# Optimization experiments

Hardware: AMD Instinct MI355X
Metric: run time of the kernel (lower is better)

## Reference

```python
import jax, jax.numpy as jnp
import numpy as np

DIM = 256; DIM_HEAD = 32; HEADS = DIM // DIM_HEAD; WSZ = 8; D4 = DIM // 4
EPS = 1e-5
SCALE = DIM_HEAD ** -0.5


def _rel_pos_indices(wsz):
    pos = np.arange(wsz)
    grid = np.stack(np.meshgrid(pos, pos, indexing='ij')).reshape(2, -1).T  # (w*w, 2)
    rel = grid[:, None] - grid[None, :] + wsz - 1
    return jnp.asarray((rel * np.array([2 * wsz - 1, 1])).sum(-1))  # (w*w, w*w)


def _ln(x, g, b):
    m = x.mean(-1, keepdims=True)
    v = jnp.var(x, axis=-1, keepdims=True)
    return (x - m) / jnp.sqrt(v + EPS) * g + b


def setup_inputs() -> dict:
    key = jax.random.key(0)
    ks = jax.random.split(key, 8)
    inner = HEADS * DIM_HEAD
    def n(k, shape, s=0.02):
        return jax.random.normal(k, shape, dtype=jnp.float32) * s
    return {
        "x": jax.random.normal(ks[0], (2, DIM, 256, 256), dtype=jnp.float32),
        "norm_g": jnp.ones((1, DIM, 1, 1), jnp.float32),
        "norm_b": jnp.zeros((1, DIM, 1, 1), jnp.float32),
        "w_qkv": n(ks[1], (3 * inner, DIM)),
        "w_out": n(ks[2], (DIM, inner)),
        "b_out": jnp.zeros((DIM,), jnp.float32),
        "dpb_w1": n(ks[3], (D4, 2), 0.5), "dpb_b1": jnp.zeros((D4,), jnp.float32),
        "dpb_g1": jnp.ones((D4,), jnp.float32), "dpb_beta1": jnp.zeros((D4,), jnp.float32),
        "dpb_w2": n(ks[4], (D4, D4), 0.1), "dpb_b2": jnp.zeros((D4,), jnp.float32),
        "dpb_g2": jnp.ones((D4,), jnp.float32), "dpb_beta2": jnp.zeros((D4,), jnp.float32),
        "dpb_w3": n(ks[5], (D4, D4), 0.1), "dpb_b3": jnp.zeros((D4,), jnp.float32),
        "dpb_g3": jnp.ones((D4,), jnp.float32), "dpb_beta3": jnp.zeros((D4,), jnp.float32),
        "dpb_w4": n(ks[6], (1, D4), 0.1), "dpb_b4": jnp.zeros((1,), jnp.float32),
    }


def reference(x, norm_g, norm_b, w_qkv, w_out, b_out,
              dpb_w1, dpb_b1, dpb_g1, dpb_beta1,
              dpb_w2, dpb_b2, dpb_g2, dpb_beta2,
              dpb_w3, dpb_b3, dpb_g3, dpb_beta3,
              dpb_w4, dpb_b4):
    B, D, H, W = x.shape
    nh, nw = H // WSZ, W // WSZ
    # channel-first LayerNorm (stats over dim=1, biased variance)
    mean = x.mean(axis=1, keepdims=True)
    var = jnp.var(x, axis=1, keepdims=True)
    xn = (x - mean) / jnp.sqrt(var + EPS) * norm_g + norm_b
    # 'short' windowing: b d (h s1) (w s2) -> (b h w) d (s1 s2)
    xw = xn.reshape(B, D, nh, WSZ, nw, WSZ).transpose(0, 2, 4, 1, 3, 5)
    xw = xw.reshape(B * nh * nw, D, WSZ * WSZ)
    # 1x1 conv QKV == matmul over channel dim
    qkv = jnp.einsum('ed,bdn->ben', w_qkv, xw)
    q, k, v = jnp.split(qkv, 3, axis=1)
    to_heads = lambda t: t.reshape(-1, HEADS, DIM_HEAD, WSZ * WSZ).transpose(0, 1, 3, 2)
    q, k, v = to_heads(q) * SCALE, to_heads(k), to_heads(v)
    sim = jnp.einsum('bhid,bhjd->bhij', q, k)  # [Bw, H, 64, 64]
    # dynamic position bias MLP over relative coordinates in [-wsz, wsz]
    pos = jnp.arange(-WSZ, WSZ + 1, dtype=x.dtype)
    rel = jnp.stack(jnp.meshgrid(pos, pos, indexing='ij')).reshape(2, -1).T  # ((2w+1)^2, 2)
    h1 = jax.nn.relu(_ln(rel @ dpb_w1.T + dpb_b1, dpb_g1, dpb_beta1))
    h2 = jax.nn.relu(_ln(h1 @ dpb_w2.T + dpb_b2, dpb_g2, dpb_beta2))
    h3 = jax.nn.relu(_ln(h2 @ dpb_w3.T + dpb_b3, dpb_g3, dpb_beta3))
    biases = (h3 @ dpb_w4.T + dpb_b4)[:, 0]
    sim = sim + biases[_rel_pos_indices(WSZ)]
    attn = jax.nn.softmax(sim, axis=-1)
    out = jnp.einsum('bhij,bhjd->bhid', attn, v)
    # b h (x y) d -> b (h d) (x y)
    out = out.transpose(0, 1, 3, 2).reshape(-1, HEADS * DIM_HEAD, WSZ * WSZ)
    out = jnp.einsum('de,ben->bdn', w_out, out) + b_out[None, :, None]
    # (b h w) d s1 s2 -> b d (h s1) (w s2)
    out = out.reshape(B, nh, nw, D, WSZ, WSZ).transpose(0, 3, 1, 4, 2, 5).reshape(B, D, H, W)
    return out
```

## Files before the change

kernel.cpp:

```cpp
#include <hip/hip_runtime.h>


typedef __attribute__((ext_vector_type(8))) short bf16x8;
typedef __attribute__((ext_vector_type(4))) short bf16x4;
typedef __attribute__((ext_vector_type(4))) float f32x4;

#define LOG2E    1.44269504088896f
#define QK_SCALE 0.17677669529663687f

__device__ __forceinline__ short f2b(float f) {
  union { float f; unsigned u; } v; v.f = f;
  unsigned r = v.u + 0x7FFFu + ((v.u >> 16) & 1u);
  return (short)(r >> 16);
}

__device__ __forceinline__ unsigned pk2(float a, float b) {
  union { float f; unsigned u; } ua, ub; ua.f = a; ub.f = b;
#if __has_builtin(__builtin_amdgcn_perm)
  return __builtin_amdgcn_perm(ub.u + 0x8000u, ua.u + 0x8000u, 0x07060302u);
#else
  return ((ua.u + 0x8000u) >> 16) | ((ub.u + 0x8000u) & 0xFFFF0000u);
#endif
}

__device__ __forceinline__ bf16x8 mk8(unsigned a, unsigned b, unsigned c, unsigned d) {
  union { unsigned u[4]; bf16x8 v; } x; x.u[0] = a; x.u[1] = b; x.u[2] = c; x.u[3] = d;
  return x.v;
}
__device__ __forceinline__ bf16x4 mk4(unsigned a, unsigned b) {
  union { unsigned u[2]; bf16x4 v; } x; x.u[0] = a; x.u[1] = b; return x.v;
}

__device__ __forceinline__ f32x4 mfma16(bf16x4 a, bf16x4 b, f32x4 c) {
#if __has_builtin(__builtin_amdgcn_mfma_f32_16x16x16bf16_1k)
  return __builtin_amdgcn_mfma_f32_16x16x16bf16_1k(a, b, c, 0, 0, 0);
#else
  f32x4 d;
  asm volatile("v_mfma_f32_16x16x16_bf16 %0, %1, %2, %3"
               : "=&v"(d) : "v"(a), "v"(b), "v"(c));
  return d;
#endif
}

__device__ __forceinline__ float wave_sum64(float v) {
  v += __shfl_xor(v, 1);  v += __shfl_xor(v, 2);  v += __shfl_xor(v, 4);
  v += __shfl_xor(v, 8);  v += __shfl_xor(v, 16); v += __shfl_xor(v, 32);
  return v;
}

__global__ __launch_bounds__(256)
void prep_kernel(const float* __restrict__ wqkv, const float* __restrict__ wout,
                 const float* __restrict__ w1, const float* __restrict__ b1,
                 const float* __restrict__ g1, const float* __restrict__ be1,
                 const float* __restrict__ w2, const float* __restrict__ b2,
                 const float* __restrict__ g2, const float* __restrict__ be2,
                 const float* __restrict__ w3, const float* __restrict__ b3,
                 const float* __restrict__ g3, const float* __restrict__ be3,
                 const float* __restrict__ w4, const float* __restrict__ b4,
                 short* __restrict__ wq_t, short* __restrict__ wo_t,
                 float* __restrict__ sb) {
  __shared__ float h[64];
  __shared__ float wbuf[4096];

  if (blockIdx.x < 128) {
    int t = (blockIdx.x * 256 + threadIdx.x) * 8;
    if (t < 196608) {
      int blk = t >> 9, l = (t & 511) >> 3;
      int et = blk >> 3, kt = blk & 7;
      int e = et * 16 + (l & 15);
      int d = kt * 32 + (l >> 4) * 8;
      const float* src = wqkv + e * 256 + d;
      float sc = (e < 256) ? QK_SCALE * LOG2E : 1.0f;
      bf16x8 pk;
      #pragma unroll
      for (int el = 0; el < 8; ++el) pk[el] = f2b(src[el] * sc);
      *(bf16x8*)(wq_t + t) = pk;
    } else {
      int o = t - 196608;
      int blk = o >> 9, l = (o & 511) >> 3;
      int dt = blk >> 3, kt = blk & 7;
      int dout = dt * 16 + (l & 15);
      int e = kt * 32 + (l >> 4) * 8;
      const float* src = wout + dout * 256 + e;
      bf16x8 pk;
      #pragma unroll
      for (int el = 0; el < 8; ++el) pk[el] = f2b(src[el]);
      *(bf16x8*)(wo_t + o) = pk;
    }
    return;
  }

  if (threadIdx.x >= 64) return;
  const int f = threadIdx.x;
  const int pos = blockIdx.x - 128;
  const float py = (float)(pos / 17) - 8.0f;
  const float px = (float)(pos % 17) - 8.0f;

  float a = py * w1[2 * f] + px * w1[2 * f + 1] + b1[f];
  {
    float m = wave_sum64(a) * (1.f / 64.f);
    float d = a - m;
    float var = wave_sum64(d * d) * (1.f / 64.f);
    a = fmaxf(d * rsqrtf(var + 1e-5f) * g1[f] + be1[f], 0.f);
  }
  h[f] = a;
  __threadfence_block();

  #pragma unroll 8
  for (int k = 0; k < 64; ++k) wbuf[k * 64 + f] = w2[k * 64 + f];
  __threadfence_block();
  float acc = b2[f];
  #pragma unroll 8
  for (int k = 0; k < 64; ++k) {
    int g = (k + f) & 63;
    acc += wbuf[f * 64 + g] * h[g];
  }
  {
    float m = wave_sum64(acc) * (1.f / 64.f);
    float d = acc - m;
    float var = wave_sum64(d * d) * (1.f / 64.f);
    acc = fmaxf(d * rsqrtf(var + 1e-5f) * g2[f] + be2[f], 0.f);
  }
  __threadfence_block();
  h[f] = acc;
  __threadfence_block();

  #pragma unroll 8
  for (int k = 0; k < 64; ++k) wbuf[k * 64 + f] = w3[k * 64 + f];
  __threadfence_block();
  float acc3 = b3[f];
  #pragma unroll 8
  for (int k = 0; k < 64; ++k) {
    int g = (k + f) & 63;
    acc3 += wbuf[f * 64 + g] * h[g];
  }
  {
    float m = wave_sum64(acc3) * (1.f / 64.f);
    float d = acc3 - m;
    float var = wave_sum64(d * d) * (1.f / 64.f);
    acc3 = fmaxf(d * rsqrtf(var + 1e-5f) * g3[f] + be3[f], 0.f);
  }
  float o = wave_sum64(w4[f] * acc3);
  if (f == 0) sb[pos] = o + b4[0];
}

__global__ __launch_bounds__(512)
void expand_kernel(const float* __restrict__ sb, float* __restrict__ tblf) {
  int idx = blockIdx.x * 512 + threadIdx.x;
  int it = idx >> 10, jt = (idx >> 8) & 3, ln = (idx >> 2) & 63, jj = idx & 3;
  int rr = ln & 15, gg = ln >> 4;
  int i = it * 16 + rr;
  int j = jt * 16 + gg * 4 + jj;
  int dy = (i >> 3) - (j >> 3) + 7;
  int dx = (i & 7) - (j & 7) + 7;
  tblf[idx] = sb[dy * 15 + dx] * LOG2E;
}

#define SM_XA   0
#define SM_PS   65536
#define SM_SIZE 73728
#define XASWZ(p) ((((p) & 7) << 4) ^ ((((p) >> 3) & 3) << 7))

__global__ __launch_bounds__(512)
void attn_kernel(const float* __restrict__ x, const float* __restrict__ gnorm,
                 const float* __restrict__ bnorm, const short* __restrict__ wq_t,
                 const short* __restrict__ wo_t, const float* __restrict__ bout,
                 const float* __restrict__ tblf, float* __restrict__ out) {
  __shared__ __align__(16) char smem[SM_SIZE];
  const int t = threadIdx.x;
  const int lane = t & 63;
  const int w = t >> 6;
  const int r = lane & 15;
  const int gq = lane >> 4;

  const int bid = blockIdx.x;
  const int b   = bid >> 9;
  const int wh  = (bid >> 4) & 31;
  const int ww2 = bid & 15;
  const int R = wh * 8, C = ww2 * 16;

  const int n = lane;
  const int d0 = w * 32;
  float* PS = (float*)(smem + SM_PS);
  float xv[2][32];
  #pragma unroll
  for (int h = 0; h < 2; ++h) {
    const float* xb = x + (((size_t)(b * 256 + d0)) << 16) +
                      (R + 4 * h + (n >> 4)) * 256 + C + (n & 15);
    float s1 = 0.f, s2v = 0.f;
    #pragma unroll
    for (int i = 0; i < 32; ++i) {
      float v = xb[(size_t)i << 16];
      xv[h][i] = v; s1 += v; s2v += v * v;
    }
    PS[h * 1024 + w * 64 + n] = s1;
    PS[h * 1024 + 512 + w * 64 + n] = s2v;
  }
  __syncthreads();
  #pragma unroll
  for (int h = 0; h < 2; ++h) {
    float a = 0.f, q2 = 0.f;
    #pragma unroll
    for (int dg = 0; dg < 8; ++dg) {
      a  += PS[h * 1024 + dg * 64 + n];
      q2 += PS[h * 1024 + 512 + dg * 64 + n];
    }
    float mean = a * (1.f / 256.f);
    float var = q2 * (1.f / 256.f) - mean * mean;
    float rstd = rsqrtf(var + 1e-5f);
    int p2 = (4 * h + (n >> 4)) * 16 + (n & 15);
    #pragma unroll
    for (int c = 0; c < 4; ++c) {
      float xn[8];
      #pragma unroll
      for (int e = 0; e < 8; ++e) {
        int d = d0 + c * 8 + e;
        xn[e] = (xv[h][c * 8 + e] - mean) * rstd * gnorm[d] + bnorm[d];
      }
      *(bf16x8*)(smem + SM_XA + (p2 << 9) + ((((d0 + c * 8) << 1)) ^ XASWZ(p2))) =
          mk8(pk2(xn[0], xn[1]), pk2(xn[2], xn[3]), pk2(xn[4], xn[5]), pk2(xn[6], xn[7]));
    }
  }
  __syncthreads();

  const f32x4 vzero = {0.f, 0.f, 0.f, 0.f};

  f32x4 o2[2][2][4];
  float pinv[2][4];
  #pragma unroll
  for (int wl = 0; wl < 2; ++wl) {
    bf16x4 kpk[2][4], qpk[2][4];
    {
      f32x4 aq[2][4], ak[2][4];
      #pragma unroll
      for (int nt = 0; nt < 2; ++nt)
        #pragma unroll
        for (int t4 = 0; t4 < 4; ++t4) { aq[nt][t4] = vzero; ak[nt][t4] = vzero; }
      __builtin_amdgcn_s_setprio(1);
      #pragma unroll
      for (int kt = 0; kt < 8; ++kt) {
        bf16x8 bq0 = *(const bf16x8*)(wq_t + ((((0 * 16 + w * 2 + 0) * 8 + kt) << 9) + lane * 8));
        bf16x8 bq1 = *(const bf16x8*)(wq_t + ((((0 * 16 + w * 2 + 1) * 8 + kt) << 9) + lane * 8));
        bf16x8 bk0 = *(const bf16x8*)(wq_t + ((((1 * 16 + w * 2 + 0) * 8 + kt) << 9) + lane * 8));
        bf16x8 bk1 = *(const bf16x8*)(wq_t + ((((1 * 16 + w * 2 + 1) * 8 + kt) << 9) + lane * 8));
        bf16x8 afr[4];
        #pragma unroll
        for (int t4 = 0; t4 < 4; ++t4) {
          int p2 = (t4 * 2 + (r >> 3)) * 16 + wl * 8 + (r & 7);
          afr[t4] = *(const bf16x8*)(smem + SM_XA + (p2 << 9) + ((((kt * 32 + gq * 8) << 1)) ^ XASWZ(p2)));
        }
        #pragma unroll
        for (int t4 = 0; t4 < 4; ++t4) {
          aq[0][t4] = __builtin_amdgcn_mfma_f32_16x16x32_bf16(bq0, afr[t4], aq[0][t4], 0, 0, 0);
          aq[1][t4] = __builtin_amdgcn_mfma_f32_16x16x32_bf16(bq1, afr[t4], aq[1][t4], 0, 0, 0);
          ak[0][t4] = __builtin_amdgcn_mfma_f32_16x16x32_bf16(bk0, afr[t4], ak[0][t4], 0, 0, 0);
          ak[1][t4] = __builtin_amdgcn_mfma_f32_16x16x32_bf16(bk1, afr[t4], ak[1][t4], 0, 0, 0);
        }
      }
      __builtin_amdgcn_s_setprio(0);
      #pragma unroll
      for (int kb = 0; kb < 2; ++kb)
        #pragma unroll
        for (int t4 = 0; t4 < 4; ++t4) {
          qpk[kb][t4] = mk4(pk2(aq[kb][t4][0], aq[kb][t4][1]),
                            pk2(aq[kb][t4][2], aq[kb][t4][3]));
          kpk[kb][t4] = mk4(pk2(ak[kb][t4][0], ak[kb][t4][1]),
                            pk2(ak[kb][t4][2], ak[kb][t4][3]));
        }
    }
    bf16x4 va8[4][2];
    {
      f32x4 vacc[4][2];
      #pragma unroll
      for (int mt = 0; mt < 4; ++mt)
        #pragma unroll
        for (int nt = 0; nt < 2; ++nt) vacc[mt][nt] = vzero;
      __builtin_amdgcn_s_setprio(1);
      #pragma unroll
      for (int kt = 0; kt < 8; ++kt) {
        bf16x8 bfr0 = *(const bf16x8*)(wq_t + ((((2 * 16 + w * 2 + 0) * 8 + kt) << 9) + lane * 8));
        bf16x8 bfr1 = *(const bf16x8*)(wq_t + ((((2 * 16 + w * 2 + 1) * 8 + kt) << 9) + lane * 8));
        bf16x8 afr[4];
        #pragma unroll
        for (int mt = 0; mt < 4; ++mt) {
          int p2 = (mt * 2 + (r >> 3)) * 16 + wl * 8 + (r & 7);
          afr[mt] = *(const bf16x8*)(smem + SM_XA + (p2 << 9) + ((((kt * 32 + gq * 8) << 1)) ^ XASWZ(p2)));
        }
        #pragma unroll
        for (int mt = 0; mt < 4; ++mt) {
          vacc[mt][0] = __builtin_amdgcn_mfma_f32_16x16x32_bf16(afr[mt], bfr0, vacc[mt][0], 0, 0, 0);
          vacc[mt][1] = __builtin_amdgcn_mfma_f32_16x16x32_bf16(afr[mt], bfr1, vacc[mt][1], 0, 0, 0);
        }
      }
      __builtin_amdgcn_s_setprio(0);
      #pragma unroll
      for (int mt = 0; mt < 4; ++mt)
        #pragma unroll
        for (int nt = 0; nt < 2; ++nt)
          va8[mt][nt] = mk4(pk2(vacc[mt][nt][0], vacc[mt][nt][1]),
                            pk2(vacc[mt][nt][2], vacc[mt][nt][3]));
    }

    #pragma unroll
    for (int nt = 0; nt < 2; ++nt)
      #pragma unroll
      for (int it = 0; it < 4; ++it) o2[wl][nt][it] = vzero;
    __builtin_amdgcn_s_setprio(1);
    #pragma unroll
    for (int it = 0; it < 4; ++it) {
      f32x4 sc[4];
      #pragma unroll
      for (int jt = 0; jt < 4; ++jt) {
        sc[jt] = mfma16(kpk[0][jt], qpk[0][it], vzero);
        sc[jt] = mfma16(kpk[1][jt], qpk[1][it], sc[jt]);
      }
      float sum = 0.f;
      #pragma unroll
      for (int jt = 0; jt < 4; ++jt) {
        f32x4 bj = *(const f32x4*)(tblf + (((it * 4 + jt) * 64 + lane) << 2));
        #pragma unroll
        for (int jj = 0; jj < 4; ++jj) {
          float e = exp2f(sc[jt][jj] + bj[jj]);
          sc[jt][jj] = e; sum += e;
        }
      }
      sum += __shfl_xor(sum, 16);
      sum += __shfl_xor(sum, 32);
      pinv[wl][it] = 1.0f / sum;
      bf16x4 ppk[4];
      #pragma unroll
      for (int jt = 0; jt < 4; ++jt)
        ppk[jt] = mk4(pk2(sc[jt][0], sc[jt][1]), pk2(sc[jt][2], sc[jt][3]));
      #pragma unroll
      for (int mt = 0; mt < 4; ++mt)
        #pragma unroll
        for (int nt = 0; nt < 2; ++nt)
          o2[wl][nt][it] = mfma16(va8[mt][nt], ppk[mt], o2[wl][nt][it]);
    }
    __builtin_amdgcn_s_setprio(0);
  }
  __syncthreads();

  float bov[2];
  bov[0] = bout[w * 32 + r];
  bov[1] = bout[w * 32 + 16 + r];
  bf16x8 woB[2][8];
  #pragma unroll
  for (int nt = 0; nt < 2; ++nt)
    #pragma unroll
    for (int kt = 0; kt < 8; ++kt)
      woB[nt][kt] = *(const bf16x8*)(wo_t + ((((w * 2 + nt) * 8 + kt) << 9) + lane * 8));

  #pragma unroll
  for (int wl = 0; wl < 2; ++wl)
    #pragma unroll
    for (int nt = 0; nt < 2; ++nt)
      #pragma unroll
      for (int it = 0; it < 4; ++it) {
        float pv = pinv[wl][it];
        int pw = it * 16 + r;
        int p2 = ((pw >> 3) << 4) + (wl << 3) + (pw & 7);
        int e = (w << 5) + (nt << 4) + (gq << 2);
        *(bf16x4*)(smem + SM_XA + (p2 << 9) + (((e << 1)) ^ XASWZ(p2))) =
            mk4(pk2(o2[wl][nt][it][0] * pv, o2[wl][nt][it][1] * pv),
                pk2(o2[wl][nt][it][2] * pv, o2[wl][nt][it][3] * pv));
      }
  __syncthreads();

  #pragma unroll 1
  for (int ck = 0; ck < 2; ++ck) {
    f32x4 c3[4][2];
    #pragma unroll
    for (int mt = 0; mt < 4; ++mt)
      #pragma unroll
      for (int nt = 0; nt < 2; ++nt) c3[mt][nt] = vzero;
    __builtin_amdgcn_s_setprio(1);
    #pragma unroll
    for (int kt = 0; kt < 8; ++kt) {
      bf16x8 af[4];
      #pragma unroll
      for (int mt = 0; mt < 4; ++mt) {
        int p2 = ck * 64 + mt * 16 + r;
        af[mt] = *(const bf16x8*)(smem + SM_XA + (p2 << 9) + ((((kt * 32 + gq * 8) << 1)) ^ XASWZ(p2)));
      }
      #pragma unroll
      for (int mt = 0; mt < 4; ++mt)
        #pragma unroll
        for (int nt = 0; nt < 2; ++nt)
          c3[mt][nt] = __builtin_amdgcn_mfma_f32_16x16x32_bf16(af[mt], woB[nt][kt], c3[mt][nt], 0, 0, 0);
    }
    __builtin_amdgcn_s_setprio(0);
    #pragma unroll
    for (int mt = 0; mt < 4; ++mt)
      #pragma unroll
      for (int nt = 0; nt < 2; ++nt) {
        int dout = w * 32 + nt * 16 + r;
        int row = ck * 4 + mt;
        f32x4 v = c3[mt][nt];
        v[0] += bov[nt]; v[1] += bov[nt]; v[2] += bov[nt]; v[3] += bov[nt];
        *(f32x4*)(out + (((size_t)(b * 256 + dout)) << 16) + (R + row) * 256 + C + gq * 4) = v;
      }
  }
}

extern "C" void kernel_launch(void* const* d_in, const int* in_sizes, int n_in,
                              void* d_out, int out_size, void* d_ws, size_t ws_size,
                              hipStream_t stream) {
  const float* x     = (const float*)d_in[0];
  const float* gnorm = (const float*)d_in[1];
  const float* bnorm = (const float*)d_in[2];
  const float* wqkv  = (const float*)d_in[3];
  const float* wout  = (const float*)d_in[4];
  const float* bout  = (const float*)d_in[5];
  const float* w1  = (const float*)d_in[6];
  const float* b1  = (const float*)d_in[7];
  const float* g1  = (const float*)d_in[8];
  const float* be1 = (const float*)d_in[9];
  const float* w2  = (const float*)d_in[10];
  const float* b2  = (const float*)d_in[11];
  const float* g2  = (const float*)d_in[12];
  const float* be2 = (const float*)d_in[13];
  const float* w3  = (const float*)d_in[14];
  const float* b3  = (const float*)d_in[15];
  const float* g3  = (const float*)d_in[16];
  const float* be3 = (const float*)d_in[17];
  const float* w4  = (const float*)d_in[18];
  const float* b4  = (const float*)d_in[19];

  short* wq_t = (short*)d_ws;
  short* wo_t = wq_t + 196608;
  float* sb   = (float*)((char*)d_ws + 524288);
  float* tblf = (float*)((char*)d_ws + 528384);

  prep_kernel<<<dim3(417), dim3(256), 0, stream>>>(
      wqkv, wout, w1, b1, g1, be1, w2, b2, g2, be2, w3, b3, g3, be3, w4, b4,
      wq_t, wo_t, sb);
  expand_kernel<<<dim3(8), dim3(512), 0, stream>>>(sb, tblf);

  attn_kernel<<<dim3(1024), dim3(512), 0, stream>>>(
      x, gnorm, bnorm, wq_t, wo_t, bout, tblf, (float*)d_out);
}
```

Measured before the change: 167.1 us.

## Split QKV projection from attention and interleave two windows in softmax stage

Measured after the change: 201.7 us. +20.7%, slower.

```diff
diff --git a/kernel.cpp b/kernel.cpp
--- a/kernel.cpp
+++ b/kernel.cpp
@@ -225,120 +225,133 @@
 
   const f32x4 vzero = {0.f, 0.f, 0.f, 0.f};
 
+  bf16x4 qpk[2][2][4], kpk[2][2][4];
+  #pragma unroll 1
+  for (int wl = 0; wl < 2; ++wl) {
+    f32x4 aq[2][4], ak[2][4];
+    #pragma unroll
+    for (int nt = 0; nt < 2; ++nt)
+      #pragma unroll
+      for (int t4 = 0; t4 < 4; ++t4) { aq[nt][t4] = vzero; ak[nt][t4] = vzero; }
+    __builtin_amdgcn_s_setprio(1);
+    #pragma unroll
+    for (int kt = 0; kt < 8; ++kt) {
+      bf16x8 bq0 = *(const bf16x8*)(wq_t + ((((0 * 16 + w * 2 + 0) * 8 + kt) << 9) + lane * 8));
+      bf16x8 bq1 = *(const bf16x8*)(wq_t + ((((0 * 16 + w * 2 + 1) * 8 + kt) << 9) + lane * 8));
+      bf16x8 bk0 = *(const bf16x8*)(wq_t + ((((1 * 16 + w * 2 + 0) * 8 + kt) << 9) + lane * 8));
+      bf16x8 bk1 = *(const bf16x8*)(wq_t + ((((1 * 16 + w * 2 + 1) * 8 + kt) << 9) + lane * 8));
+      bf16x8 afr[4];
+      #pragma unroll
+      for (int t4 = 0; t4 < 4; ++t4) {
+        int p2 = (t4 * 2 + (r >> 3)) * 16 + wl * 8 + (r & 7);
+        afr[t4] = *(const bf16x8*)(smem + SM_XA + (p2 << 9) + ((((kt * 32 + gq * 8) << 1)) ^ XASWZ(p2)));
+      }
+      #pragma unroll
+      for (int t4 = 0; t4 < 4; ++t4) {
+        aq[0][t4] = __builtin_amdgcn_mfma_f32_16x16x32_bf16(bq0, afr[t4], aq[0][t4], 0, 0, 0);
+        aq[1][t4] = __builtin_amdgcn_mfma_f32_16x16x32_bf16(bq1, afr[t4], aq[1][t4], 0, 0, 0);
+        ak[0][t4] = __builtin_amdgcn_mfma_f32_16x16x32_bf16(bk0, afr[t4], ak[0][t4], 0, 0, 0);
+        ak[1][t4] = __builtin_amdgcn_mfma_f32_16x16x32_bf16(bk1, afr[t4], ak[1][t4], 0, 0, 0);
+      }
+    }
+    __builtin_amdgcn_s_setprio(0);
+    #pragma unroll
+    for (int kb = 0; kb < 2; ++kb)
+      #pragma unroll
+      for (int t4 = 0; t4 < 4; ++t4) {
+        qpk[wl][kb][t4] = mk4(pk2(aq[kb][t4][0], aq[kb][t4][1]),
+                              pk2(aq[kb][t4][2], aq[kb][t4][3]));
+        kpk[wl][kb][t4] = mk4(pk2(ak[kb][t4][0], ak[kb][t4][1]),
+                              pk2(ak[kb][t4][2], ak[kb][t4][3]));
+      }
+  }
+
+  bf16x4 va8[2][4][2];
+  #pragma unroll 1
+  for (int wl = 0; wl < 2; ++wl) {
+    f32x4 vacc[4][2];
+    #pragma unroll
+    for (int mt = 0; mt < 4; ++mt)
+      #pragma unroll
+      for (int nt = 0; nt < 2; ++nt) vacc[mt][nt] = vzero;
+    __builtin_amdgcn_s_setprio(1);
+    #pragma unroll
+    for (int kt = 0; kt < 8; ++kt) {
+      bf16x8 bfr0 = *(const bf16x8*)(wq_t + ((((2 * 16 + w * 2 + 0) * 8 + kt) << 9) + lane * 8));
+      bf16x8 bfr1 = *(const bf16x8*)(wq_t + ((((2 * 16 + w * 2 + 1) * 8 + kt) << 9) + lane * 8));
+      bf16x8 afr[4];
+      #pragma unroll
+      for (int mt = 0; mt < 4; ++mt) {
+        int p2 = (mt * 2 + (r >> 3)) * 16 + wl * 8 + (r & 7);
+        afr[mt] = *(const bf16x8*)(smem + SM_XA + (p2 << 9) + ((((kt * 32 + gq * 8) << 1)) ^ XASWZ(p2)));
+      }
+      #pragma unroll
+      for (int mt = 0; mt < 4; ++mt) {
+        vacc[mt][0] = __builtin_amdgcn_mfma_f32_16x16x32_bf16(afr[mt], bfr0, vacc[mt][0], 0, 0, 0);
+        vacc[mt][1] = __builtin_amdgcn_mfma_f32_16x16x32_bf16(afr[mt], bfr1, vacc[mt][1], 0, 0, 0);
+      }
+    }
+    __builtin_amdgcn_s_setprio(0);
+    #pragma unroll
+    for (int mt = 0; mt < 4; ++mt)
+      #pragma unroll
+      for (int nt = 0; nt < 2; ++nt)
+        va8[wl][mt][nt] = mk4(pk2(vacc[mt][nt][0], vacc[mt][nt][1]),
+                              pk2(vacc[mt][nt][2], vacc[mt][nt][3]));
+  }
+
   f32x4 o2[2][2][4];
   float pinv[2][4];
   #pragma unroll
-  for (int wl = 0; wl < 2; ++wl) {
-    bf16x4 kpk[2][4], qpk[2][4];
-    {
-      f32x4 aq[2][4], ak[2][4];
-      #pragma unroll
-      for (int nt = 0; nt < 2; ++nt)
-        #pragma unroll
-        for (int t4 = 0; t4 < 4; ++t4) { aq[nt][t4] = vzero; ak[nt][t4] = vzero; }
-      __builtin_amdgcn_s_setprio(1);
-      #pragma unroll
-      for (int kt = 0; kt < 8; ++kt) {
-        bf16x8 bq0 = *(const bf16x8*)(wq_t + ((((0 * 16 + w * 2 + 0) * 8 + kt) << 9) + lane * 8));
-        bf16x8 bq1 = *(const bf16x8*)(wq_t + ((((0 * 16 + w * 2 + 1) * 8 + kt) << 9) + lane * 8));
-        bf16x8 bk0 = *(const bf16x8*)(wq_t + ((((1 * 16 + w * 2 + 0) * 8 + kt) << 9) + lane * 8));
-        bf16x8 bk1 = *(const bf16x8*)(wq_t + ((((1 * 16 + w * 2 + 1) * 8 + kt) << 9) + lane * 8));
-        bf16x8 afr[4];
-        #pragma unroll
-        for (int t4 = 0; t4 < 4; ++t4) {
-          int p2 = (t4 * 2 + (r >> 3)) * 16 + wl * 8 + (r & 7);
-          afr[t4] = *(const bf16x8*)(smem + SM_XA + (p2 << 9) + ((((kt * 32 + gq * 8) << 1)) ^ XASWZ(p2)));
-        }
-        #pragma unroll
-        for (int t4 = 0; t4 < 4; ++t4) {
-          aq[0][t4] = __builtin_amdgcn_mfma_f32_16x16x32_bf16(bq0, afr[t4], aq[0][t4], 0, 0, 0);
-          aq[1][t4] = __builtin_amdgcn_mfma_f32_16x16x32_bf16(bq1, afr[t4], aq[1][t4], 0, 0, 0);
-          ak[0][t4] = __builtin_amdgcn_mfma_f32_16x16x32_bf16(bk0, afr[t4], ak[0][t4], 0, 0, 0);
-          ak[1][t4] = __builtin_amdgcn_mfma_f32_16x16x32_bf16(bk1, afr[t4], ak[1][t4], 0, 0, 0);
-        }
-      }
-      __builtin_amdgcn_s_setprio(0);
-      #pragma unroll
-      for (int kb = 0; kb < 2; ++kb)
-        #pragma unroll
-        for (int t4 = 0; t4 < 4; ++t4) {
-          qpk[kb][t4] = mk4(pk2(aq[kb][t4][0], aq[kb][t4][1]),
-                            pk2(aq[kb][t4][2], aq[kb][t4][3]));
-          kpk[kb][t4] = mk4(pk2(ak[kb][t4][0], ak[kb][t4][1]),
-                            pk2(ak[kb][t4][2], ak[kb][t4][3]));
-        }
-    }
-    bf16x4 va8[4][2];
-    {
-      f32x4 vacc[4][2];
-      #pragma unroll
-      for (int mt = 0; mt < 4; ++mt)
-        #pragma unroll
-        for (int nt = 0; nt < 2; ++nt) vacc[mt][nt] = vzero;
-      __builtin_amdgcn_s_setprio(1);
-      #pragma unroll
-      for (int kt = 0; kt < 8; ++kt) {
-        bf16x8 bfr0 = *(const bf16x8*)(wq_t + ((((2 * 16 + w * 2 + 0) * 8 + kt) << 9) + lane * 8));
-        bf16x8 bfr1 = *(const bf16x8*)(wq_t + ((((2 * 16 + w * 2 + 1) * 8 + kt) << 9) + lane * 8));
-        bf16x8 afr[4];
-        #pragma unroll
-        for (int mt = 0; mt < 4; ++mt) {
-          int p2 = (mt * 2 + (r >> 3)) * 16 + wl * 8 + (r & 7);
-          afr[mt] = *(const bf16x8*)(smem + SM_XA + (p2 << 9) + ((((kt * 32 + gq * 8) << 1)) ^ XASWZ(p2)));
-        }
-        #pragma unroll
-        for (int mt = 0; mt < 4; ++mt) {
-          vacc[mt][0] = __builtin_amdgcn_mfma_f32_16x16x32_bf16(afr[mt], bfr0, vacc[mt][0], 0, 0, 0);
-          vacc[mt][1] = __builtin_amdgcn_mfma_f32_16x16x32_bf16(afr[mt], bfr1, vacc[mt][1], 0, 0, 0);
-        }
-      }
-      __builtin_amdgcn_s_setprio(0);
+  for (int wl = 0; wl < 2; ++wl)
+    #pragma unroll
+    for (int nt = 0; nt < 2; ++nt)
+      #pragma unroll
+      for (int it = 0; it < 4; ++it) o2[wl][nt][it] = vzero;
+  __builtin_amdgcn_s_setprio(1);
+  #pragma unroll
+  for (int it = 0; it < 4; ++it) {
+    f32x4 sc[2][4];
+    #pragma unroll
+    for (int wl = 0; wl < 2; ++wl)
+      #pragma unroll
+      for (int jt = 0; jt < 4; ++jt) {
+        sc[wl][jt] = mfma16(kpk[wl][0][jt], qpk[wl][0][it], vzero);
+        sc[wl][jt] = mfma16(kpk[wl][1][jt], qpk[wl][1][it], sc[wl][jt]);
+      }
+    float sum0 = 0.f, sum1 = 0.f;
+    #pragma unroll
+    for (int jt = 0; jt < 4; ++jt) {
+      f32x4 bj = *(const f32x4*)(tblf + (((it * 4 + jt) * 64 + lane) << 2));
+      #pragma unroll
+      for (int jj = 0; jj < 4; ++jj) {
+        float e0 = exp2f(sc[0][jt][jj] + bj[jj]);
+        float e1 = exp2f(sc[1][jt][jj] + bj[jj]);
+        sc[0][jt][jj] = e0; sum0 += e0;
+        sc[1][jt][jj] = e1; sum1 += e1;
+      }
+    }
+    sum0 += __shfl_xor(sum0, 16);
+    sum1 += __shfl_xor(sum1, 16);
+    sum0 += __shfl_xor(sum0, 32);
+    sum1 += __shfl_xor(sum1, 32);
+    pinv[0][it] = 1.0f / sum0;
+    pinv[1][it] = 1.0f / sum1;
+    #pragma unroll
+    for (int wl = 0; wl < 2; ++wl) {
+      bf16x4 ppk[4];
+      #pragma unroll
+      for (int jt = 0; jt < 4; ++jt)
+        ppk[jt] = mk4(pk2(sc[wl][jt][0], sc[wl][jt][1]),
+                      pk2(sc[wl][jt][2], sc[wl][jt][3]));
       #pragma unroll
       for (int mt = 0; mt < 4; ++mt)
         #pragma unroll
         for (int nt = 0; nt < 2; ++nt)
-          va8[mt][nt] = mk4(pk2(vacc[mt][nt][0], vacc[mt][nt][1]),
-                            pk2(vacc[mt][nt][2], vacc[mt][nt][3]));
-    }
-
-    #pragma unroll
-    for (int nt = 0; nt < 2; ++nt)
-      #pragma unroll
-      for (int it = 0; it < 4; ++it) o2[wl][nt][it] = vzero;
-    __builtin_amdgcn_s_setprio(1);
-    #pragma unroll
-    for (int it = 0; it < 4; ++it) {
-      f32x4 sc[4];
-      #pragma unroll
-      for (int jt = 0; jt < 4; ++jt) {
-        sc[jt] = mfma16(kpk[0][jt], qpk[0][it], vzero);
-        sc[jt] = mfma16(kpk[1][jt], qpk[1][it], sc[jt]);
-      }
-      float sum = 0.f;
-      #pragma unroll
-      for (int jt = 0; jt < 4; ++jt) {
-        f32x4 bj = *(const f32x4*)(tblf + (((it * 4 + jt) * 64 + lane) << 2));
-        #pragma unroll
-        for (int jj = 0; jj < 4; ++jj) {
-          float e = exp2f(sc[jt][jj] + bj[jj]);
-          sc[jt][jj] = e; sum += e;
-        }
-      }
-      sum += __shfl_xor(sum, 16);
-      sum += __shfl_xor(sum, 32);
-      pinv[wl][it] = 1.0f / sum;
-      bf16x4 ppk[4];
-      #pragma unroll
-      for (int jt = 0; jt < 4; ++jt)
-        ppk[jt] = mk4(pk2(sc[jt][0], sc[jt][1]), pk2(sc[jt][2], sc[jt][3]));
-      #pragma unroll
-      for (int mt = 0; mt < 4; ++mt)
-        #pragma unroll
-        for (int nt = 0; nt < 2; ++nt)
-          o2[wl][nt][it] = mfma16(va8[mt][nt], ppk[mt], o2[wl][nt][it]);
-    }
-    __builtin_amdgcn_s_setprio(0);
-  }
+          o2[wl][nt][it] = mfma16(va8[wl][mt][nt], ppk[mt], o2[wl][nt][it]);
+    }
+  }
+  __builtin_amdgcn_s_setprio(0);
   __syncthreads();
 
   float bov[2];
```
